# Kernel tuning notes

Hardware: AMD Instinct MI355X
Metric: run time of the kernel (lower is better)

The kernel has to match this reference:

```python
import jax, jax.numpy as jnp
import numpy as np

D = 512        # latent_dim
CD = D // 2    # complex_dim = 256
R = 8          # low-rank
UD = 32        # u_dim
NY = 50        # n_y = 2*num_prod + num_inj
SEL_IN = D + UD + 1
H = 128
EPS = 1e-5


def _bn_relu(x, g, b):
    # BatchNorm1d (training mode: batch stats, biased var) + ReLU
    mu = jnp.mean(x, axis=0)
    var = jnp.mean((x - mu) ** 2, axis=0)
    return jax.nn.relu((x - mu) / jnp.sqrt(var + EPS) * g + b)


_LAYERS = [("0", SEL_IN, H), ("1", H, H), ("2", H, D),
           ("a", D, CD), ("o", D, CD),
           ("Ur", D, CD * R), ("Ui", D, CD * R),
           ("Vr", D, CD * R), ("Vi", D, CD * R),
           ("Br", D, CD * UD), ("Bi", D, CD * UD),
           ("Cr", D, NY * CD), ("Ci", D, NY * CD),
           ("D", D, NY * UD)]


def setup_inputs() -> dict:
    key = jax.random.key(0)
    B = 2048
    inp = {}
    k0, k1, k2, kp = jax.random.split(key, 4)
    inp["zt"] = jax.random.normal(k0, (B, D), jnp.float32)
    inp["dt"] = jax.random.uniform(k1, (B, 1), jnp.float32)
    inp["ut"] = jax.random.normal(k2, (B, UD), jnp.float32)
    ks = jax.random.split(kp, len(_LAYERS))
    for (name, fin, fout), k in zip(_LAYERS, ks):
        kw, kb = jax.random.split(k)
        inp["W" + name] = jax.random.normal(kw, (fin, fout), jnp.float32) * 0.02
        inp["b" + name] = jax.random.normal(kb, (fout,), jnp.float32) * 0.02
    # BN affine params for the two hidden selector layers
    inp["g0"] = jnp.ones((H,), jnp.float32)
    inp["be0"] = jnp.zeros((H,), jnp.float32)
    inp["g1"] = jnp.ones((H,), jnp.float32)
    inp["be1"] = jnp.zeros((H,), jnp.float32)
    return inp


def _fwd(zt, dt, ut, W0, b0, g0, be0, W1, b1, g1, be1, W2, b2,
         Wa, ba, Wo, bo, WUr, bUr, WUi, bUi, WVr, bVr, WVi, bVi,
         WBr, bBr, WBi, bBi, WCr, bCr, WCi, bCi, WD, bD):
    B = zt.shape[0]
    z = jax.lax.complex(zt[:, :CD], zt[:, CD:])               # [B, CD] complex
    x = jnp.concatenate([zt, ut, dt], axis=-1)                # [B, SEL_IN]
    h = _bn_relu(x @ W0 + b0, g0, be0)
    h = _bn_relu(h @ W1 + b1, g1, be1)
    hz = h @ W2 + b2                                          # [B, D]

    alpha = -jax.nn.softplus(hz @ Wa + ba)                    # [B, CD]
    omega = hz @ Wo + bo
    Lam = jnp.exp(jax.lax.complex(alpha, omega))              # |Lam| < 1

    U = jax.lax.complex(hz @ WUr + bUr, hz @ WUi + bUi).reshape(B, CD, R)
    V = jax.lax.complex(hz @ WVr + bVr, hz @ WVi + bVi).reshape(B, CD, R)
    # U (V^H z): [B, CD]
    t = jnp.einsum('bdr,bd->br', jnp.conj(V), z)
    low_rank = jnp.einsum('bdr,br->bd', U, t)

    Bt = jax.lax.complex(hz @ WBr + bBr, hz @ WBi + bBi).reshape(B, CD, UD)
    ut_dt = ut * dt                                           # [B, UD] real
    ut_dt_c = ut_dt.astype(Lam.dtype)
    z_next = Lam * z + low_rank + jnp.einsum('bdu,bu->bd', Bt, ut_dt_c)

    Ct = jax.lax.complex(hz @ WCr + bCr, hz @ WCi + bCi).reshape(B, NY, CD)
    Dt = (hz @ WD + bD).reshape(B, NY, UD)
    yt = jnp.einsum('bnd,bd->bn', Ct, z_next).real + jnp.einsum('bnu,bu->bn', Dt, ut_dt)

    z_next_real = jnp.concatenate([z_next.real, z_next.imag], axis=-1)  # [B, D]
    return z_next_real, yt


def reference(zt, dt, ut, W0, b0, g0, be0, W1, b1, g1, be1, W2, b2,
              Wa, ba, Wo, bo, WUr, bUr, WUi, bUi, WVr, bVr, WVi, bVi,
              WBr, bBr, WBi, bBi, WCr, bCr, WCi, bCi, WD, bD):
    return _fwd(zt, dt, ut, W0, b0, g0, be0, W1, b1, g1, be1, W2, b2,
                Wa, ba, Wo, bo, WUr, bUr, WUi, bUi, WVr, bVr, WVi, bVi,
                WBr, bBr, WBi, bBi, WCr, bCr, WCi, bCi, WD, bD)
```

## Files before the change

### kernel.cpp

```cpp
#include <hip/hip_runtime.h>
#include <hip/hip_bf16.h>
#include <cstdint>
#include <cstddef>


typedef __bf16 bf16;
typedef __bf16 bf16x8 __attribute__((ext_vector_type(8)));
typedef __bf16 bf16x4 __attribute__((ext_vector_type(4)));
typedef float f32x4 __attribute__((ext_vector_type(4)));

__device__ __forceinline__ void async16(const void* g, void* l) {
  __builtin_amdgcn_global_load_lds((const __attribute__((address_space(1))) void*)g,
                                   (__attribute__((address_space(3))) void*)l, 16, 0, 0);
}

__device__ __forceinline__ bool tile_map(int NT, int& m0, int& n0) {
  int L = blockIdx.x;
  int x = L & 7, s = L >> 3;
  int nt = ((s >> 4) << 3) + x;
  if (nt >= NT) return false;
  n0 = nt << 7;
  m0 = (s & 15) << 7;
  return true;
}

__device__ __forceinline__ void gemm_p3(const bf16* __restrict__ A,
                                        const bf16* __restrict__ Bw,
                                        int m0, int n0,
                                        bf16* lds, f32x4 acc[4][4]) {
  const int tid = threadIdx.x;
  const int w = tid >> 6, l = tid & 63;
  const int wm = (w >> 1) << 6, wn = (w & 1) << 6;
  const int fr = l & 15, q = l >> 4;

  const int c0 = tid, c1 = tid + 256;
  const int r0 = c0 >> 2, k0 = ((c0 & 3) ^ ((r0 >> 1) & 3)) << 3;
  const int r1 = c1 >> 2, k1 = ((c1 & 3) ^ ((r1 >> 1) & 3)) << 3;
  const bf16* a0 = A + (size_t)(m0 + r0) * 512 + k0;
  const bf16* a1 = A + (size_t)(m0 + r1) * 512 + k1;
  const bf16* b0 = Bw + (size_t)(n0 + r0) * 512 + k0;
  const bf16* b1 = Bw + (size_t)(n0 + r1) * 512 + k1;
  const int sw = (q ^ ((fr >> 1) & 3)) << 3;

#pragma unroll
  for (int mt = 0; mt < 4; ++mt)
#pragma unroll
    for (int nt = 0; nt < 4; ++nt) { f32x4 z = {0.f, 0.f, 0.f, 0.f}; acc[mt][nt] = z; }

  auto issue = [&](int kt, int p) {
    bf16* d = lds + p * 8192;
    async16(a0 + kt, d + (c0 << 3));
    async16(a1 + kt, d + (c1 << 3));
    async16(b0 + kt, d + 4096 + (c0 << 3));
    async16(b1 + kt, d + 4096 + (c1 << 3));
  };

  issue(0, 0);
  issue(32, 1);
#pragma unroll
  for (int it = 0; it < 16; ++it) {
    const int p = it % 3;
    if (it < 14) asm volatile("s_waitcnt vmcnt(4)" ::: "memory");
    else         asm volatile("s_waitcnt vmcnt(0)" ::: "memory");
    asm volatile("s_barrier" ::: "memory");
    const bf16* ab = lds + p * 8192;
    const bf16* bb = ab + 4096;
    bf16x8 af[4], bfv[4];
#pragma unroll
    for (int mt = 0; mt < 4; ++mt)
      af[mt] = *(const bf16x8*)(ab + (wm + mt * 16 + fr) * 32 + sw);
#pragma unroll
    for (int nt = 0; nt < 4; ++nt)
      bfv[nt] = *(const bf16x8*)(bb + (wn + nt * 16 + fr) * 32 + sw);
    asm volatile("s_waitcnt lgkmcnt(0)" ::: "memory");
    if (it + 2 < 16) issue((it + 2) << 5, (it + 2) % 3);
#pragma unroll
    for (int mt = 0; mt < 4; ++mt)
#pragma unroll
      for (int nt = 0; nt < 4; ++nt)
        acc[mt][nt] = __builtin_amdgcn_mfma_f32_16x16x32_bf16(af[mt], bfv[nt],
                                                              acc[mt][nt], 0, 0, 0);
  }
}

struct TEntry { const float* src; bf16* dst; int N, tile0, ntn; };
struct TArgs { TEntry e[11]; };

__global__ void k_transpose(TArgs a) {
  __shared__ float tile[64][65];
  int t = blockIdx.x;
  int ei = 0;
  while (ei < 10 && t >= a.e[ei + 1].tile0) ++ei;
  const TEntry E = a.e[ei];
  int lt = t - E.tile0;
  int tk = lt / E.ntn, tn = lt - tk * E.ntn;
  int k0 = tk << 6, n0 = tn << 6;
  int tid = threadIdx.x;
#pragma unroll
  for (int i = 0; i < 4; ++i) {
    int idx = tid + i * 256;
    int kk = idx >> 4, c4 = (idx & 15) << 2;
    const float4 v = *(const float4*)(E.src + (size_t)(k0 + kk) * E.N + n0 + c4);
    tile[c4 + 0][kk] = v.x; tile[c4 + 1][kk] = v.y;
    tile[c4 + 2][kk] = v.z; tile[c4 + 3][kk] = v.w;
  }
  __syncthreads();
#pragma unroll
  for (int i = 0; i < 4; ++i) {
    int idx = tid + i * 256;
    int nn = idx >> 4, k4 = (idx & 15) << 2;
    bf16x4 o;
    o[0] = (bf16)tile[nn][k4 + 0]; o[1] = (bf16)tile[nn][k4 + 1];
    o[2] = (bf16)tile[nn][k4 + 2]; o[3] = (bf16)tile[nn][k4 + 3];
    *(bf16x4*)(E.dst + (size_t)(n0 + nn) * 512 + k0 + k4) = o;
  }
}

__global__ void k_prep(const float* ba, const float* bo, const float* bVr, const float* bVi,
                       const float* bBr, const float* bBi, const float* bD,
                       const float* bUr, const float* bUi, const float* bCr, const float* bCi,
                       float* bbigA, float* bbigB, float* bbigC) {
  int i = blockIdx.x * 256 + threadIdx.x;
  if (i < 22656) {
    float v;
    if (i < 256) v = ba[i];
    else if (i < 512) v = bo[i - 256];
    else if (i < 2560) v = bVr[i - 512];
    else if (i < 4608) v = bVi[i - 2560];
    else if (i < 12800) v = bBr[i - 4608];
    else if (i < 20992) v = bBi[i - 12800];
    else if (i < 22592) v = bD[i - 20992];
    else v = 0.f;
    bbigA[i] = v;
  }
  int j = i - 22656;
  if (j >= 0 && j < 4096) bbigB[j] = (j < 2048) ? bUr[j] : bUi[j - 2048];
  int m = i - (22656 + 4096);
  if (m >= 0 && m < 25600) bbigC[m] = (m < 12800) ? bCr[m] : bCi[m - 12800];
}

__global__ void k_lin0(const float* __restrict__ zt, const float* __restrict__ dt,
                       const float* __restrict__ ut, const float* __restrict__ W0,
                       const float* __restrict__ b0, float* __restrict__ s0) {
  int i = blockIdx.x * 256 + threadIdx.x;
  int b = i >> 7, c = i & 127;
  const float* w = W0 + c;
  const float* x = zt + (size_t)b * 512;
  float acc = b0[c];
#pragma unroll 4
  for (int k = 0; k < 512; ++k) acc = fmaf(x[k], w[(size_t)k * 128], acc);
  const float* u = ut + (size_t)b * 32;
#pragma unroll
  for (int k = 0; k < 32; ++k) acc = fmaf(u[k], w[(size_t)(512 + k) * 128], acc);
  acc = fmaf(dt[b], w[(size_t)544 * 128], acc);
  s0[i] = acc;
}

__global__ void k_stats(const float* __restrict__ s, float* __restrict__ mu,
                        float* __restrict__ rstd) {
  int c = blockIdx.x;
  float sm = 0.f, sq = 0.f;
  for (int r = threadIdx.x; r < 2048; r += 256) {
    float v = s[(size_t)r * 128 + c];
    sm += v; sq += v * v;
  }
#pragma unroll
  for (int o = 32; o >= 1; o >>= 1) { sm += __shfl_down(sm, o); sq += __shfl_down(sq, o); }
  __shared__ float red[8];
  int w = threadIdx.x >> 6;
  if ((threadIdx.x & 63) == 0) { red[w] = sm; red[4 + w] = sq; }
  __syncthreads();
  if (threadIdx.x == 0) {
    float S = red[0] + red[1] + red[2] + red[3];
    float Q = red[4] + red[5] + red[6] + red[7];
    float m = S * (1.f / 2048.f);
    float var = Q * (1.f / 2048.f) - m * m;
    mu[c] = m;
    rstd[c] = rsqrtf(var + 1e-5f);
  }
}

__global__ void k_lin1(const float* __restrict__ s0, const float* __restrict__ mu,
                       const float* __restrict__ rstd, const float* __restrict__ g,
                       const float* __restrict__ be, const float* __restrict__ W1,
                       const float* __restrict__ b1, float* __restrict__ s1) {
  int i = blockIdx.x * 256 + threadIdx.x;
  int b = i >> 7, c = i & 127;
  const float* w = W1 + c;
  const float* x = s0 + (size_t)b * 128;
  float acc = b1[c];
#pragma unroll 4
  for (int k = 0; k < 128; ++k) {
    float h = fmaxf(fmaf((x[k] - mu[k]) * rstd[k], g[k], be[k]), 0.f);
    acc = fmaf(h, w[(size_t)k * 128], acc);
  }
  s1[i] = acc;
}

__global__ void k_lin2(const float* __restrict__ s1, const float* __restrict__ mu,
                       const float* __restrict__ rstd, const float* __restrict__ g,
                       const float* __restrict__ be, const float* __restrict__ W2,
                       const float* __restrict__ b2, bf16* __restrict__ hz) {
  int i = blockIdx.x * 256 + threadIdx.x;
  int b = i >> 9, c = i & 511;
  const float* w = W2 + c;
  const float* x = s1 + (size_t)b * 128;
  float acc = b2[c];
#pragma unroll 4
  for (int k = 0; k < 128; ++k) {
    float h = fmaxf(fmaf((x[k] - mu[k]) * rstd[k], g[k], be[k]), 0.f);
    acc = fmaf(h, w[(size_t)k * 512], acc);
  }
  hz[i] = (bf16)acc;
}

__global__ __launch_bounds__(256) void k_gemmA(
    const bf16* __restrict__ hz, const bf16* __restrict__ WT, const float* __restrict__ bias,
    const float* __restrict__ zt, const float* __restrict__ dt, const float* __restrict__ ut,
    float* __restrict__ pa, float* __restrict__ po,
    float* __restrict__ Bzr, float* __restrict__ Bzi,
    float* __restrict__ tbuf, float* __restrict__ ytout) {
  int m0, n0;
  if (!tile_map(177, m0, n0)) return;
  __shared__ __align__(16) bf16 lds[24576];
  f32x4 acc[4][4];
  gemm_p3(hz, WT, m0, n0, lds, acc);
  const int l = threadIdx.x & 63, w = threadIdx.x >> 6;
  const int wm = (w >> 1) << 6, wn = (w & 1) << 6;
  const int fr = l & 15, quad = l >> 4;
  const int ncol = n0 + wn;

  if (n0 < 512) {
    float* dst = (n0 < 256) ? pa : po;
    int cb = ncol - ((n0 < 256) ? 0 : 256);
#pragma unroll
    for (int mt = 0; mt < 4; ++mt)
#pragma unroll
      for (int j = 0; j < 4; ++j) {
        int b = m0 + wm + mt * 16 + quad * 4 + j;
#pragma unroll
        for (int nt = 0; nt < 4; ++nt) {
          int n = ncol + nt * 16 + fr;
          dst[(size_t)b * 256 + (cb + nt * 16 + fr)] = acc[mt][nt][j] + bias[n];
        }
      }
  } else if (n0 < 4608) {
    const bool isVr = n0 < 2560;
#pragma unroll
    for (int mt = 0; mt < 4; ++mt)
#pragma unroll
      for (int j = 0; j < 4; ++j) {
        int b = m0 + wm + mt * 16 + quad * 4 + j;
        float cre = 0.f, cim = 0.f;
#pragma unroll
        for (int nt = 0; nt < 4; ++nt) {
          int n = ncol + nt * 16 + fr;
          float v = acc[mt][nt][j] + bias[n];
          int d = ((n - 512) & 2047) >> 3;
          float zr = zt[(size_t)b * 512 + d], zi = zt[(size_t)b * 512 + 256 + d];
          if (isVr) { cre += v * zr; cim += v * zi; }
          else      { cre += v * zi; cim -= v * zr; }
        }
        cre += __shfl_xor(cre, 8);
        cim += __shfl_xor(cim, 8);
        if ((l & 8) == 0) {
          int r = fr & 7;
          atomicAdd(&tbuf[((size_t)b * 8 + r) * 2 + 0], cre);
          atomicAdd(&tbuf[((size_t)b * 8 + r) * 2 + 1], cim);
        }
      }
  } else if (n0 < 20992) {
    const bool isBr = n0 < 12800;
    float* dst = isBr ? Bzr : Bzi;
#pragma unroll
    for (int mt = 0; mt < 4; ++mt)
#pragma unroll
      for (int j = 0; j < 4; ++j) {
        int b = m0 + wm + mt * 16 + quad * 4 + j;
        float dtb = dt[b];
#pragma unroll
        for (int g = 0; g < 2; ++g) {
          float s = 0.f;
#pragma unroll
          for (int h = 0; h < 2; ++h) {
            int nt = g * 2 + h;
            int n = ncol + nt * 16 + fr;
            int base = (n - 4608) & 8191;
            float v = acc[mt][nt][j] + bias[n];
            s += v * ut[(size_t)b * 32 + (base & 31)];
          }
          s *= dtb;
          s += __shfl_xor(s, 1); s += __shfl_xor(s, 2);
          s += __shfl_xor(s, 4); s += __shfl_xor(s, 8);
          if ((l & 15) == 0) {
            int d = (((ncol + g * 32) - 4608) & 8191) >> 5;
            dst[(size_t)b * 256 + d] = s;
          }
        }
      }
  } else {
#pragma unroll
    for (int mt = 0; mt < 4; ++mt)
#pragma unroll
      for (int j = 0; j < 4; ++j) {
        int b = m0 + wm + mt * 16 + quad * 4 + j;
        float dtb = dt[b];
#pragma unroll
        for (int g = 0; g < 2; ++g) {
          float s = 0.f;
#pragma unroll
          for (int h = 0; h < 2; ++h) {
            int nt = g * 2 + h;
            int n = ncol + nt * 16 + fr;
            int base = n - 20992;
            float v = acc[mt][nt][j] + bias[n];
            s += v * ut[(size_t)b * 32 + (base & 31)];
          }
          s *= dtb;
          s += __shfl_xor(s, 1); s += __shfl_xor(s, 2);
          s += __shfl_xor(s, 4); s += __shfl_xor(s, 8);
          int nn = ((ncol + g * 32) - 20992) >> 5;
          if ((l & 15) == 0 && nn < 50) ytout[(size_t)b * 50 + nn] = s;
        }
      }
  }
}

__global__ __launch_bounds__(256) void k_gemmB(
    const bf16* __restrict__ hz, const bf16* __restrict__ WT, const float* __restrict__ bias,
    const float* __restrict__ tbuf, float* __restrict__ lr) {
  int m0, n0;
  if (!tile_map(32, m0, n0)) return;
  __shared__ __align__(16) bf16 lds[24576];
  f32x4 acc[4][4];
  gemm_p3(hz, WT, m0, n0, lds, acc);
  const int l = threadIdx.x & 63, w = threadIdx.x >> 6;
  const int wm = (w >> 1) << 6, wn = (w & 1) << 6;
  const int fr = l & 15, quad = l >> 4;
  const int ncol = n0 + wn;
  const bool isUr = n0 < 2048;
#pragma unroll
  for (int mt = 0; mt < 4; ++mt)
#pragma unroll
    for (int j = 0; j < 4; ++j) {
      int b = m0 + wm + mt * 16 + quad * 4 + j;
#pragma unroll
      for (int nt = 0; nt < 4; ++nt) {
        int n = ncol + nt * 16 + fr;
        int base = n & 2047;
        int r = base & 7, d = base >> 3;
        float v = acc[mt][nt][j] + bias[n];
        float tre = tbuf[((size_t)b * 8 + r) * 2], tim = tbuf[((size_t)b * 8 + r) * 2 + 1];
        float cre = isUr ? v * tre : -v * tim;
        float cim = isUr ? v * tim :  v * tre;
        cre += __shfl_xor(cre, 1); cre += __shfl_xor(cre, 2); cre += __shfl_xor(cre, 4);
        cim += __shfl_xor(cim, 1); cim += __shfl_xor(cim, 2); cim += __shfl_xor(cim, 4);
        if ((l & 7) == 0) {
          atomicAdd(&lr[((size_t)b * 256 + d) * 2 + 0], cre);
          atomicAdd(&lr[((size_t)b * 256 + d) * 2 + 1], cim);
        }
      }
    }
}

__global__ void k_assembleZ(const float* __restrict__ zt, const float* __restrict__ pa,
                            const float* __restrict__ po, const float* __restrict__ Bzr,
                            const float* __restrict__ Bzi, const float* __restrict__ lr,
                            float* __restrict__ zout, float* __restrict__ znr,
                            float* __restrict__ zni) {
  int i = blockIdx.x * 256 + threadIdx.x;
  int b = i >> 8, d = i & 255;
  float a = pa[i], o = po[i];
  float sp = fmaxf(a, 0.f) + log1pf(expf(-fabsf(a)));
  float mag = expf(-sp);
  float Lr = mag * cosf(o), Li = mag * sinf(o);
  float zr = zt[(size_t)b * 512 + d], zi = zt[(size_t)b * 512 + 256 + d];
  float re = fmaf(Lr, zr, -Li * zi) + Bzr[i] + lr[2 * i];
  float im = fmaf(Lr, zi,  Li * zr) + Bzi[i] + lr[2 * i + 1];
  zout[(size_t)b * 512 + d] = re;
  zout[(size_t)b * 512 + 256 + d] = im;
  znr[i] = re; zni[i] = im;
}

__global__ __launch_bounds__(256) void k_gemmC(
    const bf16* __restrict__ hz, const bf16* __restrict__ WT, const float* __restrict__ bias,
    const float* __restrict__ znr, const float* __restrict__ zni, float* __restrict__ ytout) {
  int m0, n0;
  if (!tile_map(200, m0, n0)) return;
  __shared__ __align__(16) bf16 lds[24576];
  f32x4 acc[4][4];
  gemm_p3(hz, WT, m0, n0, lds, acc);
  const int l = threadIdx.x & 63, w = threadIdx.x >> 6;
  const int wm = (w >> 1) << 6, wn = (w & 1) << 6;
  const int fr = l & 15, quad = l >> 4;
  const int ncol = n0 + wn;
  const bool isCr = n0 < 12800;
  const int nb = ncol - (isCr ? 0 : 12800);
  const int nn = nb >> 8;
#pragma unroll
  for (int mt = 0; mt < 4; ++mt)
#pragma unroll
    for (int j = 0; j < 4; ++j) {
      int b = m0 + wm + mt * 16 + quad * 4 + j;
      float s = 0.f;
#pragma unroll
      for (int nt = 0; nt < 4; ++nt) {
        int n = ncol + nt * 16 + fr;
        int d = (nb + nt * 16 + fr) & 255;
        float v = acc[mt][nt][j] + bias[n];
        s += isCr ? v * znr[(size_t)b * 256 + d] : -(v * zni[(size_t)b * 256 + d]);
      }
      s += __shfl_xor(s, 1); s += __shfl_xor(s, 2);
      s += __shfl_xor(s, 4); s += __shfl_xor(s, 8);
      if ((l & 15) == 0) atomicAdd(&ytout[(size_t)b * 50 + nn], s);
    }
}

extern "C" void kernel_launch(void* const* d_in, const int* in_sizes, int n_in,
                              void* d_out, int out_size, void* d_ws, size_t ws_size,
                              hipStream_t stream) {
  (void)in_sizes; (void)n_in; (void)out_size; (void)ws_size;
  const float* zt  = (const float*)d_in[0];
  const float* dt  = (const float*)d_in[1];
  const float* ut  = (const float*)d_in[2];
  const float* W0  = (const float*)d_in[3];  const float* b0  = (const float*)d_in[4];
  const float* W1  = (const float*)d_in[5];  const float* b1  = (const float*)d_in[6];
  const float* W2  = (const float*)d_in[7];  const float* b2  = (const float*)d_in[8];
  const float* Wa  = (const float*)d_in[9];  const float* ba  = (const float*)d_in[10];
  const float* Wo  = (const float*)d_in[11]; const float* bo  = (const float*)d_in[12];
  const float* WUr = (const float*)d_in[13]; const float* bUr = (const float*)d_in[14];
  const float* WUi = (const float*)d_in[15]; const float* bUi = (const float*)d_in[16];
  const float* WVr = (const float*)d_in[17]; const float* bVr = (const float*)d_in[18];
  const float* WVi = (const float*)d_in[19]; const float* bVi = (const float*)d_in[20];
  const float* WBr = (const float*)d_in[21]; const float* bBr = (const float*)d_in[22];
  const float* WBi = (const float*)d_in[23]; const float* bBi = (const float*)d_in[24];
  const float* WCr = (const float*)d_in[25]; const float* bCr = (const float*)d_in[26];
  const float* WCi = (const float*)d_in[27]; const float* bCi = (const float*)d_in[28];
  const float* WD  = (const float*)d_in[29]; const float* bD  = (const float*)d_in[30];
  const float* g0  = (const float*)d_in[31]; const float* be0 = (const float*)d_in[32];
  const float* g1  = (const float*)d_in[33]; const float* be1 = (const float*)d_in[34];

  char* ws = (char*)d_ws;
  bf16*  WTbig = (bf16*)(ws + 0);
  bf16*  WTU   = (bf16*)(ws + 23199744);
  bf16*  WTC   = (bf16*)(ws + 27394048);
  bf16*  hz    = (bf16*)(ws + 53608448);
  float* s0    = (float*)(ws + 55705600);
  float* s1    = (float*)(ws + 56754176);
  float* mu0   = (float*)(ws + 57802752);
  float* rstd0 = mu0 + 128;
  float* mu1   = mu0 + 256;
  float* rstd1 = mu0 + 384;
  float* bbigA = (float*)(ws + 57804800);
  float* bbigB = (float*)(ws + 57895424);
  float* bbigC = (float*)(ws + 57911808);
  float* pa    = (float*)(ws + 58014208);
  float* po    = (float*)(ws + 60111360);
  float* Bzr   = (float*)(ws + 62208512);
  float* Bzi   = (float*)(ws + 64305664);
  float* tbuf  = (float*)(ws + 66402816);
  float* lr    = (float*)(ws + 66533888);
  float* znr   = (float*)(ws + 70728192);
  float* zni   = (float*)(ws + 72825344);
  float* zout  = (float*)d_out;
  float* ytout = zout + 2048 * 512;

  k_prep<<<205, 256, 0, stream>>>(ba, bo, bVr, bVi, bBr, bBi, bD, bUr, bUi, bCr, bCi,
                                  bbigA, bbigB, bbigC);

  TArgs ta; int tile0 = 0; int idx = 0;
  auto add = [&](const float* src, bf16* dst, int N) {
    int ntn = N >> 6;
    ta.e[idx].src = src; ta.e[idx].dst = dst; ta.e[idx].N = N;
    ta.e[idx].tile0 = tile0; ta.e[idx].ntn = ntn;
    tile0 += ntn * 8; ++idx;
  };
  add(Wa,  WTbig + (size_t)0 * 512,     256);
  add(Wo,  WTbig + (size_t)256 * 512,   256);
  add(WVr, WTbig + (size_t)512 * 512,   2048);
  add(WVi, WTbig + (size_t)2560 * 512,  2048);
  add(WBr, WTbig + (size_t)4608 * 512,  8192);
  add(WBi, WTbig + (size_t)12800 * 512, 8192);
  add(WD,  WTbig + (size_t)20992 * 512, 1600);
  add(WUr, WTU,                         2048);
  add(WUi, WTU + (size_t)2048 * 512,    2048);
  add(WCr, WTC,                         12800);
  add(WCi, WTC + (size_t)12800 * 512,   12800);
  k_transpose<<<tile0, 256, 0, stream>>>(ta);

  hipMemsetAsync(tbuf, 0, 131072, stream);
  hipMemsetAsync(lr, 0, 4194304, stream);

  k_lin0<<<1024, 256, 0, stream>>>(zt, dt, ut, W0, b0, s0);
  k_stats<<<128, 256, 0, stream>>>(s0, mu0, rstd0);
  k_lin1<<<1024, 256, 0, stream>>>(s0, mu0, rstd0, g0, be0, W1, b1, s1);
  k_stats<<<128, 256, 0, stream>>>(s1, mu1, rstd1);
  k_lin2<<<4096, 256, 0, stream>>>(s1, mu1, rstd1, g1, be1, W2, b2, hz);

  k_gemmA<<<184 * 16, 256, 0, stream>>>(hz, WTbig, bbigA, zt, dt, ut,
                                        pa, po, Bzr, Bzi, tbuf, ytout);
  k_gemmB<<<32 * 16, 256, 0, stream>>>(hz, WTU, bbigB, tbuf, lr);
  k_assembleZ<<<2048, 256, 0, stream>>>(zt, pa, po, Bzr, Bzi, lr, zout, znr, zni);
  k_gemmC<<<200 * 16, 256, 0, stream>>>(hz, WTC, bbigC, znr, zni, ytout);
}
```

Before: 591.2 us.

## Reorder GEMM prefetch issue, split BN-normalize into own kernel, multi-accumulator FMA

After: 561.9 us. 5.0% less time.

```diff
diff --git a/kernel.cpp b/kernel.cpp
--- a/kernel.cpp
+++ b/kernel.cpp
@@ -63,6 +63,7 @@
     if (it < 14) asm volatile("s_waitcnt vmcnt(4)" ::: "memory");
     else         asm volatile("s_waitcnt vmcnt(0)" ::: "memory");
     asm volatile("s_barrier" ::: "memory");
+    if (it + 2 < 16) issue((it + 2) << 5, (it + 2) % 3);
     const bf16* ab = lds + p * 8192;
     const bf16* bb = ab + 4096;
     bf16x8 af[4], bfv[4];
@@ -72,14 +73,13 @@
 #pragma unroll
     for (int nt = 0; nt < 4; ++nt)
       bfv[nt] = *(const bf16x8*)(bb + (wn + nt * 16 + fr) * 32 + sw);
-    asm volatile("s_waitcnt lgkmcnt(0)" ::: "memory");
-    if (it + 2 < 16) issue((it + 2) << 5, (it + 2) % 3);
 #pragma unroll
     for (int mt = 0; mt < 4; ++mt)
 #pragma unroll
       for (int nt = 0; nt < 4; ++nt)
         acc[mt][nt] = __builtin_amdgcn_mfma_f32_16x16x32_bf16(af[mt], bfv[nt],
                                                               acc[mt][nt], 0, 0, 0);
+    asm volatile("s_waitcnt lgkmcnt(0)" ::: "memory");
   }
 }
 
@@ -146,14 +146,24 @@
   int b = i >> 7, c = i & 127;
   const float* w = W0 + c;
   const float* x = zt + (size_t)b * 512;
-  float acc = b0[c];
+  float a0 = b0[c], a1 = 0.f, a2 = 0.f, a3 = 0.f;
 #pragma unroll 4
-  for (int k = 0; k < 512; ++k) acc = fmaf(x[k], w[(size_t)k * 128], acc);
+  for (int k = 0; k < 512; k += 4) {
+    a0 = fmaf(x[k + 0], w[(size_t)(k + 0) * 128], a0);
+    a1 = fmaf(x[k + 1], w[(size_t)(k + 1) * 128], a1);
+    a2 = fmaf(x[k + 2], w[(size_t)(k + 2) * 128], a2);
+    a3 = fmaf(x[k + 3], w[(size_t)(k + 3) * 128], a3);
+  }
   const float* u = ut + (size_t)b * 32;
 #pragma unroll
-  for (int k = 0; k < 32; ++k) acc = fmaf(u[k], w[(size_t)(512 + k) * 128], acc);
-  acc = fmaf(dt[b], w[(size_t)544 * 128], acc);
-  s0[i] = acc;
+  for (int k = 0; k < 32; k += 4) {
+    a0 = fmaf(u[k + 0], w[(size_t)(512 + k + 0) * 128], a0);
+    a1 = fmaf(u[k + 1], w[(size_t)(512 + k + 1) * 128], a1);
+    a2 = fmaf(u[k + 2], w[(size_t)(512 + k + 2) * 128], a2);
+    a3 = fmaf(u[k + 3], w[(size_t)(512 + k + 3) * 128], a3);
+  }
+  a0 = fmaf(dt[b], w[(size_t)544 * 128], a0);
+  s0[i] = (a0 + a1) + (a2 + a3);
 }
 
 __global__ void k_stats(const float* __restrict__ s, float* __restrict__ mu,
@@ -180,38 +190,46 @@
   }
 }
 
-__global__ void k_lin1(const float* __restrict__ s0, const float* __restrict__ mu,
+__global__ void k_norm(float* __restrict__ s, const float* __restrict__ mu,
                        const float* __restrict__ rstd, const float* __restrict__ g,
-                       const float* __restrict__ be, const float* __restrict__ W1,
+                       const float* __restrict__ be) {
+  int i = blockIdx.x * 256 + threadIdx.x;
+  int c = i & 127;
+  s[i] = fmaxf(fmaf((s[i] - mu[c]) * rstd[c], g[c], be[c]), 0.f);
+}
+
+__global__ void k_lin1(const float* __restrict__ h0, const float* __restrict__ W1,
                        const float* __restrict__ b1, float* __restrict__ s1) {
   int i = blockIdx.x * 256 + threadIdx.x;
   int b = i >> 7, c = i & 127;
   const float* w = W1 + c;
-  const float* x = s0 + (size_t)b * 128;
-  float acc = b1[c];
+  const float* x = h0 + (size_t)b * 128;
+  float a0 = b1[c], a1 = 0.f, a2 = 0.f, a3 = 0.f;
 #pragma unroll 4
-  for (int k = 0; k < 128; ++k) {
-    float h = fmaxf(fmaf((x[k] - mu[k]) * rstd[k], g[k], be[k]), 0.f);
-    acc = fmaf(h, w[(size_t)k * 128], acc);
-  }
-  s1[i] = acc;
-}
-
-__global__ void k_lin2(const float* __restrict__ s1, const float* __restrict__ mu,
-                       const float* __restrict__ rstd, const float* __restrict__ g,
-                       const float* __restrict__ be, const float* __restrict__ W2,
+  for (int k = 0; k < 128; k += 4) {
+    a0 = fmaf(x[k + 0], w[(size_t)(k + 0) * 128], a0);
+    a1 = fmaf(x[k + 1], w[(size_t)(k + 1) * 128], a1);
+    a2 = fmaf(x[k + 2], w[(size_t)(k + 2) * 128], a2);
+    a3 = fmaf(x[k + 3], w[(size_t)(k + 3) * 128], a3);
+  }
+  s1[i] = (a0 + a1) + (a2 + a3);
+}
+
+__global__ void k_lin2(const float* __restrict__ h1, const float* __restrict__ W2,
                        const float* __restrict__ b2, bf16* __restrict__ hz) {
   int i = blockIdx.x * 256 + threadIdx.x;
   int b = i >> 9, c = i & 511;
   const float* w = W2 + c;
-  const float* x = s1 + (size_t)b * 128;
-  float acc = b2[c];
+  const float* x = h1 + (size_t)b * 128;
+  float a0 = b2[c], a1 = 0.f, a2 = 0.f, a3 = 0.f;
 #pragma unroll 4
-  for (int k = 0; k < 128; ++k) {
-    float h = fmaxf(fmaf((x[k] - mu[k]) * rstd[k], g[k], be[k]), 0.f);
-    acc = fmaf(h, w[(size_t)k * 512], acc);
-  }
-  hz[i] = (bf16)acc;
+  for (int k = 0; k < 128; k += 4) {
+    a0 = fmaf(x[k + 0], w[(size_t)(k + 0) * 512], a0);
+    a1 = fmaf(x[k + 1], w[(size_t)(k + 1) * 512], a1);
+    a2 = fmaf(x[k + 2], w[(size_t)(k + 2) * 512], a2);
+    a3 = fmaf(x[k + 3], w[(size_t)(k + 3) * 512], a3);
+  }
+  hz[i] = (bf16)((a0 + a1) + (a2 + a3));
 }
 
 __global__ __launch_bounds__(256) void k_gemmA(
@@ -493,9 +511,11 @@
 
   k_lin0<<<1024, 256, 0, stream>>>(zt, dt, ut, W0, b0, s0);
   k_stats<<<128, 256, 0, stream>>>(s0, mu0, rstd0);
-  k_lin1<<<1024, 256, 0, stream>>>(s0, mu0, rstd0, g0, be0, W1, b1, s1);
+  k_norm<<<1024, 256, 0, stream>>>(s0, mu0, rstd0, g0, be0);
+  k_lin1<<<1024, 256, 0, stream>>>(s0, W1, b1, s1);
   k_stats<<<128, 256, 0, stream>>>(s1, mu1, rstd1);
-  k_lin2<<<4096, 256, 0, stream>>>(s1, mu1, rstd1, g1, be1, W2, b2, hz);
+  k_norm<<<1024, 256, 0, stream>>>(s1, mu1, rstd1, g1, be1);
+  k_lin2<<<4096, 256, 0, stream>>>(s1, W2, b2, hz);
 
   k_gemmA<<<184 * 16, 256, 0, stream>>>(hz, WTbig, bbigA, zt, dt, ut,
                                         pa, po, Bzr, Bzi, tbuf, ytout);
```
